# Kernel optimization log

Measured on AMD Instinct MI355X. Metric: run time of the kernel, lower is better.

## Reference

```python
import jax, jax.numpy as jnp
import numpy as np

BN_EPS = 1e-3  # Keras BatchNormalization default epsilon


def batchnorm(x, gamma, beta):
    # axis=2 channel BN with training=True: batch stats over (batch, seq)
    m = jnp.mean(x, axis=(0, 1))
    v = jnp.var(x, axis=(0, 1))
    return gamma * (x - m) * jax.lax.rsqrt(v + BN_EPS) + beta


def setup_inputs() -> dict:
    key = jax.random.key(0)
    ks = jax.random.split(key, 8)
    B, L, Din, D, S = 8, 512, 64, 1024, 2
    s = 0.02
    return {
        "x": jax.random.normal(ks[0], (B, L, Din), jnp.float32),
        "W_embed": jax.random.normal(ks[1], (Din, D), jnp.float32) * s,
        "bn1_gamma": jnp.ones((D,), jnp.float32),
        "bn1_beta": jnp.zeros((D,), jnp.float32),
        "Wq": jax.random.normal(ks[2], (S, D, D), jnp.float32) * s,
        "bq": jnp.zeros((S, D), jnp.float32),
        "Wk": jax.random.normal(ks[3], (S, D, D), jnp.float32) * s,
        "bk": jnp.zeros((S, D), jnp.float32),
        "Wv": jax.random.normal(ks[4], (S, D, D), jnp.float32) * s,
        "bv": jnp.zeros((S, D), jnp.float32),
        "bn_gamma": jnp.ones((S, D), jnp.float32),
        "bn_beta": jnp.zeros((S, D), jnp.float32),
        "Wc1": jax.random.normal(ks[5], (S, D, D), jnp.float32) * s,
        "bc1": jnp.zeros((S, D), jnp.float32),
        "bn2_gamma": jnp.ones((S, D), jnp.float32),
        "bn2_beta": jnp.zeros((S, D), jnp.float32),
        "num_heads": 16,
    }


def reference(x, W_embed, bn1_gamma, bn1_beta, Wq, bq, Wk, bk, Wv, bv,
              bn_gamma, bn_beta, Wc1, bc1, bn2_gamma, bn2_beta, num_heads):
    # embedding: kernel-1 conv1d == matmul, then BN (training stats)
    enc = batchnorm(jnp.einsum('bli,id->bld', x, W_embed), bn1_gamma, bn1_beta)
    S = Wq.shape[0]
    B, L, D = enc.shape
    h = num_heads
    dh = D // h
    scale = 1.0 / (dh ** 0.5)
    for i in range(S):
        # relu-activated Q/K/V projections (Dense(..., activation=relu))
        q = jax.nn.relu(jnp.einsum('bld,de->ble', enc, Wq[i]) + bq[i])
        k = jax.nn.relu(jnp.einsum('bld,de->ble', enc, Wk[i]) + bk[i])
        v = jax.nn.relu(jnp.einsum('bld,de->ble', enc, Wv[i]) + bv[i])
        # split/concat head trick == reshape to [B, L, h, dh]
        qh = q.reshape(B, L, h, dh)
        kh = k.reshape(B, L, h, dh)
        vh = v.reshape(B, L, h, dh)
        scores = jnp.einsum('blhd,bmhd->bhlm', qh, kh) * scale
        attn = jax.nn.softmax(scores, axis=-1)
        out = jnp.einsum('bhlm,bmhd->blhd', attn, vh).reshape(B, L, D)
        enc = batchnorm(out + enc, bn_gamma[i], bn_beta[i])
        # feedforward: source applies conv1 TWICE (conv2 unused) — faithful
        f = jax.nn.relu(jnp.einsum('bld,de->ble', enc, Wc1[i]) + bc1[i])
        f = jax.nn.relu(jnp.einsum('bld,de->ble', f, Wc1[i]) + bc1[i])
        enc = batchnorm(f + enc, bn2_gamma[i], bn2_beta[i])
    return enc
```

## Files before the change

kernel.cpp:

```cpp
#include <hip/hip_runtime.h>
#include <hip/hip_bf16.h>
#include <cstddef>

#define D_MODEL 1024
#define M_ROWS  4096
#define BN_EPS  1e-3f
#define C_EXP2  0.18033688011112042f

typedef __attribute__((ext_vector_type(8))) short short8;
typedef __attribute__((ext_vector_type(4))) short short4v;
typedef __attribute__((ext_vector_type(8))) unsigned short ushortx8;
typedef __attribute__((ext_vector_type(4))) float f32x4;

__device__ __forceinline__ unsigned short f2bf(float f) {
    __hip_bfloat16 h = __float2bfloat16(f);
    return *reinterpret_cast<unsigned short*>(&h);
}
__device__ __forceinline__ float bf2f(unsigned short u) {
    return __uint_as_float(((unsigned)u) << 16);
}

__global__ __launch_bounds__(256)
void embed_kernel(const float* __restrict__ A, const float* __restrict__ W,
                  unsigned short* __restrict__ Sbf, float* __restrict__ accp) {
    __shared__ float As[16][132];
    __shared__ float Bs[16][132];
    const int tid = threadIdx.x;
    const int lane = tid & 63;
    const int tx = tid & 15, ty = tid >> 4;
    const int rowBase = blockIdx.y * 128;
    const int colBase = blockIdx.x * 128;
    float acc[8][8] = {};
    for (int k0 = 0; k0 < 64; k0 += 16) {
        #pragma unroll
        for (int it = 0; it < 2; ++it) {
            int idx = tid + it * 256;
            int r = idx >> 2, c4 = (idx & 3) << 2;
            const float4 v = *reinterpret_cast<const float4*>(
                &A[(size_t)(rowBase + r) * 64 + k0 + c4]);
            As[c4 + 0][r] = v.x; As[c4 + 1][r] = v.y;
            As[c4 + 2][r] = v.z; As[c4 + 3][r] = v.w;
        }
        #pragma unroll
        for (int it = 0; it < 2; ++it) {
            int idx = tid + it * 256;
            int r = idx >> 5, c4 = (idx & 31) << 2;
            const float4 v = *reinterpret_cast<const float4*>(
                &W[(size_t)(k0 + r) * D_MODEL + colBase + c4]);
            *reinterpret_cast<float4*>(&Bs[r][c4]) = v;
        }
        __syncthreads();
        #pragma unroll
        for (int k = 0; k < 16; ++k) {
            const float4 a0 = *reinterpret_cast<const float4*>(&As[k][ty * 8]);
            const float4 a1 = *reinterpret_cast<const float4*>(&As[k][ty * 8 + 4]);
            const float4 b0 = *reinterpret_cast<const float4*>(&Bs[k][tx * 8]);
            const float4 b1 = *reinterpret_cast<const float4*>(&Bs[k][tx * 8 + 4]);
            const float a[8] = {a0.x, a0.y, a0.z, a0.w, a1.x, a1.y, a1.z, a1.w};
            const float b[8] = {b0.x, b0.y, b0.z, b0.w, b1.x, b1.y, b1.z, b1.w};
            #pragma unroll
            for (int i = 0; i < 8; ++i)
                #pragma unroll
                for (int j = 0; j < 8; ++j)
                    acc[i][j] = fmaf(a[i], b[j], acc[i][j]);
        }
        __syncthreads();
    }
    float cs[8] = {}, cq[8] = {};
    #pragma unroll
    for (int i = 0; i < 8; ++i) {
        const int row = rowBase + ty * 8 + i;
        ushortx8 ov;
        #pragma unroll
        for (int j = 0; j < 8; ++j) {
            const float s = acc[i][j];
            ov[j] = f2bf(s);
            cs[j] += s; cq[j] += s * s;
        }
        *reinterpret_cast<ushortx8*>(&Sbf[(size_t)row * D_MODEL + colBase + tx * 8]) = ov;
    }
    #pragma unroll
    for (int j = 0; j < 8; ++j) {
        cs[j] += __shfl_xor(cs[j], 16); cs[j] += __shfl_xor(cs[j], 32);
        cq[j] += __shfl_xor(cq[j], 16); cq[j] += __shfl_xor(cq[j], 32);
    }
    if (lane < 16) {
        #pragma unroll
        for (int j = 0; j < 8; ++j) {
            atomicAdd(&accp[colBase + lane * 8 + j], cs[j]);
            atomicAdd(&accp[D_MODEL + colBase + lane * 8 + j], cq[j]);
        }
    }
}

template<int MODE>
__global__ __launch_bounds__(256)
void gemm_bf16_kernel(const unsigned short* __restrict__ A,
                      const unsigned short* __restrict__ Bt,
                      const float* __restrict__ bias,
                      unsigned short* __restrict__ Cout,
                      const unsigned short* __restrict__ resid,
                      float* __restrict__ accp, int N, int Kd) {
    __shared__ unsigned short As[2][128 * 32];
    __shared__ unsigned short Bs[2][128 * 32];
    const int tid = threadIdx.x;
    const int lane = tid & 63;
    const int w = tid >> 6;
    const int wr = w >> 1, wc = w & 1;
    const int rowBase = blockIdx.y * 128;
    const int colBase = blockIdx.x * 128;

    const int chunk0 = w * 64 + lane;
    const int r0 = chunk0 >> 2;
    const int c0 = (chunk0 & 3) ^ ((r0 >> 1) & 3);
    const int chunk1 = 256 + chunk0;
    const int r1 = chunk1 >> 2;
    const int c1 = (chunk1 & 3) ^ ((r1 >> 1) & 3);
    const size_t aOff0 = (size_t)(rowBase + r0) * Kd + c0 * 8;
    const size_t aOff1 = (size_t)(rowBase + r1) * Kd + c1 * 8;
    const size_t bOff0 = (size_t)(colBase + r0) * Kd + c0 * 8;
    const size_t bOff1 = (size_t)(colBase + r1) * Kd + c1 * 8;
    const int ldsOff0 = (w * 64) * 8;
    const int ldsOff1 = (256 + w * 64) * 8;

    f32x4 acc[4][4];
    #pragma unroll
    for (int m = 0; m < 4; ++m)
        #pragma unroll
        for (int n = 0; n < 4; ++n)
            acc[m][n] = (f32x4){0.f, 0.f, 0.f, 0.f};

    #define STAGE(buf, kt) do {                                                   \
        const int k0_ = (kt) << 5;                                                \
        __builtin_amdgcn_global_load_lds(                                         \
            (const __attribute__((address_space(1))) void*)(A + aOff0 + k0_),     \
            (__attribute__((address_space(3))) void*)(&As[buf][ldsOff0]), 16, 0, 0);\
        __builtin_amdgcn_global_load_lds(                                         \
            (const __attribute__((address_space(1))) void*)(A + aOff1 + k0_),     \
            (__attribute__((address_space(3))) void*)(&As[buf][ldsOff1]), 16, 0, 0);\
        __builtin_amdgcn_global_load_lds(                                         \
            (const __attribute__((address_space(1))) void*)(Bt + bOff0 + k0_),    \
            (__attribute__((address_space(3))) void*)(&Bs[buf][ldsOff0]), 16, 0, 0);\
        __builtin_amdgcn_global_load_lds(                                         \
            (const __attribute__((address_space(1))) void*)(Bt + bOff1 + k0_),    \
            (__attribute__((address_space(3))) void*)(&Bs[buf][ldsOff1]), 16, 0, 0);\
    } while (0)

    const int NT = Kd >> 5;
    STAGE(0, 0);

    const int kb = lane >> 4;
    const int s = kb ^ ((lane >> 1) & 3);
    const int rA = wr * 64 + (lane & 15);
    const int rB = wc * 64 + (lane & 15);

    for (int t = 0; t < NT; ++t) {
        __syncthreads();
        if (t + 1 < NT) STAGE((t + 1) & 1, t + 1);
        const unsigned short* as = As[t & 1];
        const unsigned short* bs = Bs[t & 1];
        short8 a[4], b[4];
        #pragma unroll
        for (int m = 0; m < 4; ++m)
            a[m] = *(const short8*)&as[(rA + m * 16) * 32 + s * 8];
        #pragma unroll
        for (int n = 0; n < 4; ++n)
            b[n] = *(const short8*)&bs[(rB + n * 16) * 32 + s * 8];
        #pragma unroll
        for (int m = 0; m < 4; ++m)
            #pragma unroll
            for (int n = 0; n < 4; ++n)
                acc[m][n] = __builtin_amdgcn_mfma_f32_16x16x32_bf16(
                    a[m], b[n], acc[m][n], 0, 0, 0);
    }
    #undef STAGE

    const int cRow0 = rowBase + wr * 64 + (lane >> 4) * 4;
    const int cCol0 = colBase + wc * 64 + (lane & 15);
    float cs[4] = {}, cq[4] = {};
    #pragma unroll
    for (int n = 0; n < 4; ++n) {
        const int col = cCol0 + n * 16;
        const float bv = bias[col];
        #pragma unroll
        for (int m = 0; m < 4; ++m)
            #pragma unroll
            for (int r = 0; r < 4; ++r) {
                const int row = cRow0 + m * 16 + r;
                float v = fmaxf(acc[m][n][r] + bv, 0.0f);
                if (MODE == 1) {
                    v += bf2f(resid[(size_t)row * N + col]);
                    cs[n] += v; cq[n] += v * v;
                }
                Cout[(size_t)row * N + col] = f2bf(v);
            }
    }
    if (MODE == 1) {
        #pragma unroll
        for (int n = 0; n < 4; ++n) {
            cs[n] += __shfl_xor(cs[n], 16); cs[n] += __shfl_xor(cs[n], 32);
            cq[n] += __shfl_xor(cq[n], 16); cq[n] += __shfl_xor(cq[n], 32);
        }
        if (lane < 16) {
            #pragma unroll
            for (int n = 0; n < 4; ++n) {
                const int col = colBase + wc * 64 + lane + n * 16;
                atomicAdd(&accp[col], cs[n]);
                atomicAdd(&accp[D_MODEL + col], cq[n]);
            }
        }
    }
}

__global__ __launch_bounds__(256)
void transpose_cvt4_kernel(const float* __restrict__ s0, const float* __restrict__ s1,
                           const float* __restrict__ s2, const float* __restrict__ s3,
                           unsigned short* __restrict__ d0, unsigned short* __restrict__ d1,
                           unsigned short* __restrict__ d2, unsigned short* __restrict__ d3) {
    const int z = blockIdx.z;
    const float* src = (z == 0) ? s0 : (z == 1) ? s1 : (z == 2) ? s2 : s3;
    unsigned short* dst = (z == 0) ? d0 : (z == 1) ? d1 : (z == 2) ? d2 : d3;
    __shared__ float T[64][65];
    const int tid = threadIdx.x;
    const int kBase = blockIdx.y * 64;
    const int nBase = blockIdx.x * 64;
    const int rr = tid >> 4;
    const int c4 = (tid & 15) * 4;
    #pragma unroll
    for (int i = 0; i < 4; ++i) {
        const int k = i * 16 + rr;
        const float4 v = *reinterpret_cast<const float4*>(
            &src[(size_t)(kBase + k) * 1024 + nBase + c4]);
        T[k][c4] = v.x; T[k][c4 + 1] = v.y; T[k][c4 + 2] = v.z; T[k][c4 + 3] = v.w;
    }
    __syncthreads();
    #pragma unroll
    for (int i = 0; i < 4; ++i) {
        const int n = i * 16 + rr;
        ushort4 o;
        o.x = f2bf(T[c4 + 0][n]); o.y = f2bf(T[c4 + 1][n]);
        o.z = f2bf(T[c4 + 2][n]); o.w = f2bf(T[c4 + 3][n]);
        *reinterpret_cast<ushort4*>(&dst[(size_t)(nBase + n) * 1024 + kBase + c4]) = o;
    }
}

__global__ __launch_bounds__(256)
void bias_concat_kernel(const float* __restrict__ bq, const float* __restrict__ bk,
                        const float* __restrict__ bv, float* __restrict__ bqkv) {
    const int j = blockIdx.x * 256 + threadIdx.x;
    bqkv[j] = (j < 1024) ? bq[j] : (j < 2048) ? bk[j - 1024] : bv[j - 2048];
}

__global__ __launch_bounds__(256)
void attn_kernel(const unsigned short* __restrict__ QKV,
                 const unsigned short* __restrict__ Ebf,
                 unsigned short* __restrict__ Sbf,
                 float* __restrict__ accp) {
    __shared__ unsigned short Qs[128 * 64];
    __shared__ unsigned short Ks[2][64 * 64];
    __shared__ unsigned short Vt[2][64 * 72];

    const int tid = threadIdx.x;
    const int lane = tid & 63;
    const int w = tid >> 6;
    const int m = lane & 15;
    const int g = lane >> 4;
    const int l7 = lane & 7;
    const int qt = blockIdx.x, hh = blockIdx.y, bb = blockIdx.z;
    const int colB = hh * 64;
    const size_t rowQ = (size_t)bb * 512 + qt * 128;
    const size_t rowKV = (size_t)bb * 512;

    const int vk0 = (tid & 31) * 2;
    const int vcv = tid >> 5;

    #define STAGE_K(buf, kt) do {                                                  \
        const size_t kb_ = rowKV + (size_t)(kt) * 64;                              \
        _Pragma("unroll")                                                          \
        for (int i_ = 0; i_ < 2; ++i_) {                                           \
            const int c_ = w * 128 + i_ * 64 + lane;                               \
            const int r_ = c_ >> 3;                                                \
            const int gc_ = (c_ & 7) ^ (r_ & 7);                                   \
            __builtin_amdgcn_global_load_lds(                                      \
                (const __attribute__((address_space(1))) void*)                    \
                    (QKV + (kb_ + r_) * 3072 + 1024 + colB + gc_ * 8),             \
                (__attribute__((address_space(3))) void*)                          \
                    (&Ks[buf][(w * 128 + i_ * 64) * 8]), 16, 0, 0);                \
        }                                                                          \
    } while (0)

    #define LOAD_V(kt) do {                                                        \
        const size_t kb_ = rowKV + (size_t)(kt) * 64;                              \
        vst0 = *(const ushortx8*)(QKV + (kb_ + vk0) * 3072 + 2048 + colB + vcv * 8);\
        vst1 = *(const ushortx8*)(QKV + (kb_ + vk0 + 1) * 3072 + 2048 + colB + vcv * 8);\
    } while (0)

    #define WRITE_V(buf) do {                                                      \
        _Pragma("unroll")                                                          \
        for (int j_ = 0; j_ < 8; ++j_) {                                           \
            const int d_ = vcv * 8 + j_;                                           \
            unsigned int pk_ = (unsigned int)(unsigned short)vst0[j_] |            \
                               ((unsigned int)(unsigned short)vst1[j_] << 16);     \
            *(unsigned int*)&Vt[buf][d_ * 72 + vk0] = pk_;                         \
        }                                                                          \
    } while (0)

    ushortx8 vst0, vst1;

    #pragma unroll
    for (int i = 0; i < 4; ++i) {
        const int c = w * 256 + i * 64 + lane;
        const int r = c >> 3;
        const int gc = (c & 7) ^ (r & 7);
        __builtin_amdgcn_global_load_lds(
            (const __attribute__((address_space(1))) void*)
                (QKV + (rowQ + r) * 3072 + colB + gc * 8),
            (__attribute__((address_space(3))) void*)
                (&Qs[(w * 256 + i * 64) * 8]), 16, 0, 0);
    }
    STAGE_K(0, 0);
    LOAD_V(0);
    WRITE_V(0);
    __syncthreads();

    short8 qb[2][2];
    #pragma unroll
    for (int nf = 0; nf < 2; ++nf)
        #pragma unroll
        for (int ks = 0; ks < 2; ++ks)
            qb[nf][ks] = *(const short8*)&Qs[(w * 32 + 16 * nf + m) * 64 +
                                             ((g + 4 * ks) ^ l7) * 8];

    f32x4 o[2][4];
    #pragma unroll
    for (int nf = 0; nf < 2; ++nf)
        #pragma unroll
        for (int dn = 0; dn < 4; ++dn)
            o[nf][dn] = (f32x4){0.f, 0.f, 0.f, 0.f};
    float mr[2] = {-1e30f, -1e30f};
    float lsm[2] = {0.f, 0.f};

    for (int kt = 0; kt < 8; ++kt) {
        const int cur = kt & 1, nxt = cur ^ 1;
        if (kt < 7) { STAGE_K(nxt, kt + 1); LOAD_V(kt + 1); }

        f32x4 st[4][2];
        #pragma unroll
        for (int mf = 0; mf < 4; ++mf)
            #pragma unroll
            for (int nf = 0; nf < 2; ++nf)
                st[mf][nf] = (f32x4){0.f, 0.f, 0.f, 0.f};
        #pragma unroll
        for (int ks = 0; ks < 2; ++ks) {
            short8 a[4];
            #pragma unroll
            for (int mf = 0; mf < 4; ++mf)
                a[mf] = *(const short8*)&Ks[cur][(m + 16 * mf) * 64 +
                                                 ((g + 4 * ks) ^ l7) * 8];
            #pragma unroll
            for (int mf = 0; mf < 4; ++mf)
                #pragma unroll
                for (int nf = 0; nf < 2; ++nf)
                    st[mf][nf] = __builtin_amdgcn_mfma_f32_16x16x32_bf16(
                        a[mf], qb[nf][ks], st[mf][nf], 0, 0, 0);
        }

        float pmax[2];
        #pragma unroll
        for (int nf = 0; nf < 2; ++nf) {
            float mx = st[0][nf][0];
            #pragma unroll
            for (int mf = 0; mf < 4; ++mf)
                #pragma unroll
                for (int r = 0; r < 4; ++r)
                    mx = fmaxf(mx, st[mf][nf][r]);
            mx = fmaxf(mx, __shfl_xor(mx, 16));
            mx = fmaxf(mx, __shfl_xor(mx, 32));
            pmax[nf] = mx;
        }
        const int need = (pmax[0] - mr[0] > 64.f) || (pmax[1] - mr[1] > 64.f);
        if (__any(need)) {
            float al[2];
            #pragma unroll
            for (int nf = 0; nf < 2; ++nf) {
                const float mn = fmaxf(mr[nf], pmax[nf]);
                al[nf] = exp2f((mr[nf] - mn) * C_EXP2);
                lsm[nf] *= al[nf];
                mr[nf] = mn;
            }
            #pragma unroll
            for (int nf = 0; nf < 2; ++nf)
                #pragma unroll
                for (int r = 0; r < 4; ++r) {
                    const float av = __shfl(al[nf], 4 * g + r);
                    #pragma unroll
                    for (int dn = 0; dn < 4; ++dn)
                        o[nf][dn][r] *= av;
                }
        }

        float pf[2][4][4];
        #pragma unroll
        for (int nf = 0; nf < 2; ++nf) {
            const float mc = mr[nf] * C_EXP2;
            float ls = 0.f;
            #pragma unroll
            for (int mf = 0; mf < 4; ++mf)
                #pragma unroll
                for (int r = 0; r < 4; ++r) {
                    const float p = exp2f(fmaf(st[mf][nf][r], C_EXP2, -mc));
                    pf[nf][mf][r] = p;
                    ls += p;
                }
            ls += __shfl_xor(ls, 16);
            ls += __shfl_xor(ls, 32);
            lsm[nf] += ls;
        }

        if (kt < 7) WRITE_V(nxt);

        short8 pb[2][2];
        #pragma unroll
        for (int nf = 0; nf < 2; ++nf)
            #pragma unroll
            for (int ks = 0; ks < 2; ++ks)
                #pragma unroll
                for (int j = 0; j < 8; ++j)
                    pb[nf][ks][j] = (short)f2bf(pf[nf][(j >> 2) + 2 * ks][j & 3]);

        #pragma unroll
        for (int ks = 0; ks < 2; ++ks) {
            short8 vb[4];
            #pragma unroll
            for (int dn = 0; dn < 4; ++dn) {
                const int d = m + 16 * dn;
                const short4v lo = *(const short4v*)&Vt[cur][d * 72 + 4 * g + 32 * ks];
                const short4v hi = *(const short4v*)&Vt[cur][d * 72 + 4 * g + 16 + 32 * ks];
                vb[dn] = __builtin_shufflevector(lo, hi, 0, 1, 2, 3, 4, 5, 6, 7);
            }
            #pragma unroll
            for (int nf = 0; nf < 2; ++nf)
                #pragma unroll
                for (int dn = 0; dn < 4; ++dn)
                    o[nf][dn] = __builtin_amdgcn_mfma_f32_16x16x32_bf16(
                        pb[nf][ks], vb[dn], o[nf][dn], 0, 0, 0);
        }
        __syncthreads();
    }

    float cs[4] = {}, cq[4] = {};
    #pragma unroll
    for (int nf = 0; nf < 2; ++nf) {
        const float inv = 1.0f / lsm[nf];
        #pragma unroll
        for (int r = 0; r < 4; ++r) {
            const float sc = __shfl(inv, 4 * g + r);
            const size_t row = rowQ + w * 32 + 16 * nf + 4 * g + r;
            #pragma unroll
            for (int dn = 0; dn < 4; ++dn) {
                const int ch = colB + 16 * dn + m;
                const float sv = o[nf][dn][r] * sc + bf2f(Ebf[row * D_MODEL + ch]);
                Sbf[row * D_MODEL + ch] = f2bf(sv);
                cs[dn] += sv; cq[dn] += sv * sv;
            }
        }
    }
    #pragma unroll
    for (int dn = 0; dn < 4; ++dn) {
        cs[dn] += __shfl_xor(cs[dn], 16); cs[dn] += __shfl_xor(cs[dn], 32);
        cq[dn] += __shfl_xor(cq[dn], 16); cq[dn] += __shfl_xor(cq[dn], 32);
    }
    if (lane < 16) {
        #pragma unroll
        for (int dn = 0; dn < 4; ++dn) {
            atomicAdd(&accp[colB + 16 * dn + lane], cs[dn]);
            atomicAdd(&accp[D_MODEL + colB + 16 * dn + lane], cq[dn]);
        }
    }
    #undef STAGE_K
    #undef LOAD_V
    #undef WRITE_V
}

__global__ __launch_bounds__(256)
void bn_final_kernel(const float* __restrict__ accp, const float* __restrict__ gamma,
                     const float* __restrict__ beta, float* __restrict__ coef) {
    const int c = blockIdx.x * 256 + threadIdx.x;
    const float mean = accp[c] * (1.0f / 4096.0f);
    const float var = accp[D_MODEL + c] * (1.0f / 4096.0f) - mean * mean;
    const float s = gamma[c] * rsqrtf(var + BN_EPS);
    coef[c] = s;
    coef[D_MODEL + c] = beta[c] - mean * s;
}

template<bool FINAL>
__global__ __launch_bounds__(256)
void bn_apply_kernel(const unsigned short* __restrict__ S, const float* __restrict__ coef,
                     unsigned short* __restrict__ Ebf, float* __restrict__ outF) {
    const int idx = blockIdx.x * 256 + threadIdx.x;
    const int c8 = (idx & 127) << 3;
    const ushortx8 sv = *(const ushortx8*)&S[(size_t)idx * 8];
    const float4 a0 = *(const float4*)&coef[c8];
    const float4 a1 = *(const float4*)&coef[c8 + 4];
    const float4 b0 = *(const float4*)&coef[D_MODEL + c8];
    const float4 b1 = *(const float4*)&coef[D_MODEL + c8 + 4];
    const float a[8] = {a0.x, a0.y, a0.z, a0.w, a1.x, a1.y, a1.z, a1.w};
    const float b[8] = {b0.x, b0.y, b0.z, b0.w, b1.x, b1.y, b1.z, b1.w};
    float o[8];
    #pragma unroll
    for (int j = 0; j < 8; ++j) o[j] = fmaf(bf2f(sv[j]), a[j], b[j]);
    if (FINAL) {
        *reinterpret_cast<float4*>(&outF[(size_t)idx * 8]) =
            make_float4(o[0], o[1], o[2], o[3]);
        *reinterpret_cast<float4*>(&outF[(size_t)idx * 8 + 4]) =
            make_float4(o[4], o[5], o[6], o[7]);
    } else {
        ushortx8 e;
        #pragma unroll
        for (int j = 0; j < 8; ++j) e[j] = f2bf(o[j]);
        *reinterpret_cast<ushortx8*>(&Ebf[(size_t)idx * 8]) = e;
    }
}

extern "C" void kernel_launch(void* const* d_in, const int* in_sizes, int n_in,
                              void* d_out, int out_size, void* d_ws, size_t ws_size,
                              hipStream_t stream) {
    const float* x       = (const float*)d_in[0];
    const float* W_embed = (const float*)d_in[1];
    const float* bn1_g   = (const float*)d_in[2];
    const float* bn1_b   = (const float*)d_in[3];
    const float* Wq      = (const float*)d_in[4];
    const float* bq      = (const float*)d_in[5];
    const float* Wk      = (const float*)d_in[6];
    const float* bk      = (const float*)d_in[7];
    const float* Wv      = (const float*)d_in[8];
    const float* bv      = (const float*)d_in[9];
    const float* bng     = (const float*)d_in[10];
    const float* bnb     = (const float*)d_in[11];
    const float* Wc1     = (const float*)d_in[12];
    const float* bc1     = (const float*)d_in[13];
    const float* bn2g    = (const float*)d_in[14];
    const float* bn2b    = (const float*)d_in[15];

    const size_t NBUF = (size_t)M_ROWS * D_MODEL;
    char* ws = (char*)d_ws;
    float* accum = (float*)ws;
    float* coef  = accum + 5 * 2048;
    float* bqkv  = coef + 2048;
    unsigned short* Ebf   = (unsigned short*)(bqkv + 3072);
    unsigned short* Sbf   = Ebf + NBUF;
    unsigned short* QKVbf = Sbf + NBUF;
    unsigned short* F1bf  = QKVbf;
    unsigned short* Wtqkv = QKVbf + (size_t)M_ROWS * 3072;
    unsigned short* Wtc1  = Wtqkv + (size_t)3072 * 1024;
    float* outF = (float*)d_out;

    hipMemsetAsync(accum, 0, 5 * 2048 * sizeof(float), stream);

    embed_kernel<<<dim3(8, 32), 256, 0, stream>>>(x, W_embed, Sbf, accum);
    bn_final_kernel<<<4, 256, 0, stream>>>(accum, bn1_g, bn1_b, coef);
    bn_apply_kernel<false><<<2048, 256, 0, stream>>>(Sbf, coef, Ebf, nullptr);

    for (int i = 0; i < 2; ++i) {
        const size_t wo = (size_t)i * D_MODEL * D_MODEL;
        const size_t bo = (size_t)i * D_MODEL;
        float* accA = accum + (1 + 2 * i) * 2048;
        float* accF = accum + (2 + 2 * i) * 2048;

        transpose_cvt4_kernel<<<dim3(16, 16, 4), 256, 0, stream>>>(
            Wq + wo, Wk + wo, Wv + wo, Wc1 + wo,
            Wtqkv, Wtqkv + (size_t)1024 * 1024, Wtqkv + (size_t)2048 * 1024, Wtc1);
        bias_concat_kernel<<<12, 256, 0, stream>>>(bq + bo, bk + bo, bv + bo, bqkv);

        gemm_bf16_kernel<0><<<dim3(24, 32), 256, 0, stream>>>(
            Ebf, Wtqkv, bqkv, QKVbf, nullptr, nullptr, 3072, 1024);
        attn_kernel<<<dim3(4, 16, 8), 256, 0, stream>>>(QKVbf, Ebf, Sbf, accA);
        bn_final_kernel<<<4, 256, 0, stream>>>(accA, bng + bo, bnb + bo, coef);
        bn_apply_kernel<false><<<2048, 256, 0, stream>>>(Sbf, coef, Ebf, nullptr);

        gemm_bf16_kernel<0><<<dim3(8, 32), 256, 0, stream>>>(
            Ebf, Wtc1, bc1 + bo, F1bf, nullptr, nullptr, 1024, 1024);
        gemm_bf16_kernel<1><<<dim3(8, 32), 256, 0, stream>>>(
            F1bf, Wtc1, bc1 + bo, Sbf, Ebf, accF, 1024, 1024);
        bn_final_kernel<<<4, 256, 0, stream>>>(accF, bn2g + bo, bn2b + bo, coef);
        if (i == 0)
            bn_apply_kernel<false><<<2048, 256, 0, stream>>>(Sbf, coef, Ebf, nullptr);
        else
            bn_apply_kernel<true><<<2048, 256, 0, stream>>>(Sbf, coef, nullptr, outF);
    }
}
```

Before: 318.3 us.

## Consolidate launches: bf16 MFMA embed, fused BN finalize, batched weight prep

Replaces the fp32 embed GEMM with a bf16 MFMA GEMM mode (MODE 2) fed by a new prep kernel that converts x and transposes W_embed. That prep kernel also zeroes the accumulators, which removes the memset. Both layers' weights are now transposed in a single launch, the bias concat kernel is dropped by selecting q/k/v bias pointers per column in the epilogue, and the BN finalize step is folded into bn_apply. The attention kernel gains setprio around its MFMAs, tree reductions for max and sum, and packed bf16 conversion. These changes cut roughly nine launches, but the embed input is now rounded to bf16 and every bn_apply thread recomputes rsqrt.

```diff
diff --git a/kernel.cpp b/kernel.cpp
--- a/kernel.cpp
+++ b/kernel.cpp
@@ -6,6 +6,7 @@
 #define M_ROWS  4096
 #define BN_EPS  1e-3f
 #define C_EXP2  0.18033688011112042f
+#define INV_N   (1.0f / 4096.0f)
 
 typedef __attribute__((ext_vector_type(8))) short short8;
 typedef __attribute__((ext_vector_type(4))) short short4v;
@@ -19,85 +20,18 @@
 __device__ __forceinline__ float bf2f(unsigned short u) {
     return __uint_as_float(((unsigned)u) << 16);
 }
-
-__global__ __launch_bounds__(256)
-void embed_kernel(const float* __restrict__ A, const float* __restrict__ W,
-                  unsigned short* __restrict__ Sbf, float* __restrict__ accp) {
-    __shared__ float As[16][132];
-    __shared__ float Bs[16][132];
-    const int tid = threadIdx.x;
-    const int lane = tid & 63;
-    const int tx = tid & 15, ty = tid >> 4;
-    const int rowBase = blockIdx.y * 128;
-    const int colBase = blockIdx.x * 128;
-    float acc[8][8] = {};
-    for (int k0 = 0; k0 < 64; k0 += 16) {
-        #pragma unroll
-        for (int it = 0; it < 2; ++it) {
-            int idx = tid + it * 256;
-            int r = idx >> 2, c4 = (idx & 3) << 2;
-            const float4 v = *reinterpret_cast<const float4*>(
-                &A[(size_t)(rowBase + r) * 64 + k0 + c4]);
-            As[c4 + 0][r] = v.x; As[c4 + 1][r] = v.y;
-            As[c4 + 2][r] = v.z; As[c4 + 3][r] = v.w;
-        }
-        #pragma unroll
-        for (int it = 0; it < 2; ++it) {
-            int idx = tid + it * 256;
-            int r = idx >> 5, c4 = (idx & 31) << 2;
-            const float4 v = *reinterpret_cast<const float4*>(
-                &W[(size_t)(k0 + r) * D_MODEL + colBase + c4]);
-            *reinterpret_cast<float4*>(&Bs[r][c4]) = v;
-        }
-        __syncthreads();
-        #pragma unroll
-        for (int k = 0; k < 16; ++k) {
-            const float4 a0 = *reinterpret_cast<const float4*>(&As[k][ty * 8]);
-            const float4 a1 = *reinterpret_cast<const float4*>(&As[k][ty * 8 + 4]);
-            const float4 b0 = *reinterpret_cast<const float4*>(&Bs[k][tx * 8]);
-            const float4 b1 = *reinterpret_cast<const float4*>(&Bs[k][tx * 8 + 4]);
-            const float a[8] = {a0.x, a0.y, a0.z, a0.w, a1.x, a1.y, a1.z, a1.w};
-            const float b[8] = {b0.x, b0.y, b0.z, b0.w, b1.x, b1.y, b1.z, b1.w};
-            #pragma unroll
-            for (int i = 0; i < 8; ++i)
-                #pragma unroll
-                for (int j = 0; j < 8; ++j)
-                    acc[i][j] = fmaf(a[i], b[j], acc[i][j]);
-        }
-        __syncthreads();
-    }
-    float cs[8] = {}, cq[8] = {};
-    #pragma unroll
-    for (int i = 0; i < 8; ++i) {
-        const int row = rowBase + ty * 8 + i;
-        ushortx8 ov;
-        #pragma unroll
-        for (int j = 0; j < 8; ++j) {
-            const float s = acc[i][j];
-            ov[j] = f2bf(s);
-            cs[j] += s; cq[j] += s * s;
-        }
-        *reinterpret_cast<ushortx8*>(&Sbf[(size_t)row * D_MODEL + colBase + tx * 8]) = ov;
-    }
-    #pragma unroll
-    for (int j = 0; j < 8; ++j) {
-        cs[j] += __shfl_xor(cs[j], 16); cs[j] += __shfl_xor(cs[j], 32);
-        cq[j] += __shfl_xor(cq[j], 16); cq[j] += __shfl_xor(cq[j], 32);
-    }
-    if (lane < 16) {
-        #pragma unroll
-        for (int j = 0; j < 8; ++j) {
-            atomicAdd(&accp[colBase + lane * 8 + j], cs[j]);
-            atomicAdd(&accp[D_MODEL + colBase + lane * 8 + j], cq[j]);
-        }
-    }
+__device__ __forceinline__ unsigned int cvt_pk_bf16(float lo, float hi) {
+    unsigned int r;
+    asm volatile("v_cvt_pk_bf16_f32 %0, %1, %2" : "=v"(r) : "v"(lo), "v"(hi));
+    return r;
 }
 
 template<int MODE>
 __global__ __launch_bounds__(256)
 void gemm_bf16_kernel(const unsigned short* __restrict__ A,
                       const unsigned short* __restrict__ Bt,
-                      const float* __restrict__ bias,
+                      const float* __restrict__ b0, const float* __restrict__ b1,
+                      const float* __restrict__ b2,
                       unsigned short* __restrict__ Cout,
                       const unsigned short* __restrict__ resid,
                       float* __restrict__ accp, int N, int Kd) {
@@ -181,21 +115,24 @@
     #pragma unroll
     for (int n = 0; n < 4; ++n) {
         const int col = cCol0 + n * 16;
-        const float bv = bias[col];
+        float bv = 0.0f;
+        if (MODE != 2) {
+            const float* bp = (col < 1024) ? b0 : (col < 2048) ? b1 : b2;
+            bv = bp[col & 1023];
+        }
         #pragma unroll
         for (int m = 0; m < 4; ++m)
             #pragma unroll
             for (int r = 0; r < 4; ++r) {
                 const int row = cRow0 + m * 16 + r;
-                float v = fmaxf(acc[m][n][r] + bv, 0.0f);
-                if (MODE == 1) {
-                    v += bf2f(resid[(size_t)row * N + col]);
-                    cs[n] += v; cq[n] += v * v;
-                }
+                float v = acc[m][n][r];
+                if (MODE != 2) v = fmaxf(v + bv, 0.0f);
+                if (MODE == 1) v += bf2f(resid[(size_t)row * N + col]);
+                if (MODE != 0) { cs[n] += v; cq[n] += v * v; }
                 Cout[(size_t)row * N + col] = f2bf(v);
             }
     }
-    if (MODE == 1) {
+    if (MODE != 0) {
         #pragma unroll
         for (int n = 0; n < 4; ++n) {
             cs[n] += __shfl_xor(cs[n], 16); cs[n] += __shfl_xor(cs[n], 32);
@@ -213,13 +150,19 @@
 }
 
 __global__ __launch_bounds__(256)
-void transpose_cvt4_kernel(const float* __restrict__ s0, const float* __restrict__ s1,
-                           const float* __restrict__ s2, const float* __restrict__ s3,
-                           unsigned short* __restrict__ d0, unsigned short* __restrict__ d1,
-                           unsigned short* __restrict__ d2, unsigned short* __restrict__ d3) {
+void prep_weights_kernel(const float* __restrict__ Wq, const float* __restrict__ Wk,
+                         const float* __restrict__ Wv, const float* __restrict__ Wc1,
+                         unsigned short* __restrict__ Wtqkv,
+                         unsigned short* __restrict__ Wtc1) {
     const int z = blockIdx.z;
-    const float* src = (z == 0) ? s0 : (z == 1) ? s1 : (z == 2) ? s2 : s3;
-    unsigned short* dst = (z == 0) ? d0 : (z == 1) ? d1 : (z == 2) ? d2 : d3;
+    const int layer = z >> 2, typ = z & 3;
+    const size_t wo = (size_t)layer * 1048576;
+    const float* src;
+    unsigned short* dst;
+    if (typ == 0)      { src = Wq + wo;  dst = Wtqkv + layer * 3145728; }
+    else if (typ == 1) { src = Wk + wo;  dst = Wtqkv + layer * 3145728 + 1048576; }
+    else if (typ == 2) { src = Wv + wo;  dst = Wtqkv + layer * 3145728 + 2097152; }
+    else               { src = Wc1 + wo; dst = Wtc1 + layer * 1048576; }
     __shared__ float T[64][65];
     const int tid = threadIdx.x;
     const int kBase = blockIdx.y * 64;
@@ -245,10 +188,44 @@
 }
 
 __global__ __launch_bounds__(256)
-void bias_concat_kernel(const float* __restrict__ bq, const float* __restrict__ bk,
-                        const float* __restrict__ bv, float* __restrict__ bqkv) {
-    const int j = blockIdx.x * 256 + threadIdx.x;
-    bqkv[j] = (j < 1024) ? bq[j] : (j < 2048) ? bk[j - 1024] : bv[j - 2048];
+void prep_misc_kernel(const float* __restrict__ x, const float* __restrict__ Wemb,
+                      unsigned short* __restrict__ xbf,
+                      unsigned short* __restrict__ Wembt,
+                      float* __restrict__ accum) {
+    const int b = blockIdx.x;
+    const int tid = threadIdx.x;
+    if (b < 128) {
+        const size_t base = (size_t)b * 2048 + tid * 8;
+        const float4 v0 = *reinterpret_cast<const float4*>(&x[base]);
+        const float4 v1 = *reinterpret_cast<const float4*>(&x[base + 4]);
+        ushortx8 o;
+        o[0] = f2bf(v0.x); o[1] = f2bf(v0.y); o[2] = f2bf(v0.z); o[3] = f2bf(v0.w);
+        o[4] = f2bf(v1.x); o[5] = f2bf(v1.y); o[6] = f2bf(v1.z); o[7] = f2bf(v1.w);
+        *reinterpret_cast<ushortx8*>(&xbf[base]) = o;
+    } else if (b < 144) {
+        __shared__ float T[64][65];
+        const int nBase = (b - 128) * 64;
+        const int rr = tid >> 4;
+        const int c4 = (tid & 15) * 4;
+        #pragma unroll
+        for (int i = 0; i < 4; ++i) {
+            const int k = i * 16 + rr;
+            const float4 v = *reinterpret_cast<const float4*>(
+                &Wemb[(size_t)k * 1024 + nBase + c4]);
+            T[k][c4] = v.x; T[k][c4 + 1] = v.y; T[k][c4 + 2] = v.z; T[k][c4 + 3] = v.w;
+        }
+        __syncthreads();
+        #pragma unroll
+        for (int i = 0; i < 4; ++i) {
+            const int n = i * 16 + rr;
+            ushort4 o;
+            o.x = f2bf(T[c4 + 0][n]); o.y = f2bf(T[c4 + 1][n]);
+            o.z = f2bf(T[c4 + 2][n]); o.w = f2bf(T[c4 + 3][n]);
+            *reinterpret_cast<ushort4*>(&Wembt[(size_t)(nBase + n) * 64 + c4]) = o;
+        }
+    } else {
+        for (int j = tid; j < 5 * 2048; j += 256) accum[j] = 0.0f;
+    }
 }
 
 __global__ __launch_bounds__(256)
@@ -357,23 +334,28 @@
             for (int mf = 0; mf < 4; ++mf)
                 a[mf] = *(const short8*)&Ks[cur][(m + 16 * mf) * 64 +
                                                  ((g + 4 * ks) ^ l7) * 8];
+            __builtin_amdgcn_s_setprio(1);
             #pragma unroll
             for (int mf = 0; mf < 4; ++mf)
                 #pragma unroll
                 for (int nf = 0; nf < 2; ++nf)
                     st[mf][nf] = __builtin_amdgcn_mfma_f32_16x16x32_bf16(
                         a[mf], qb[nf][ks], st[mf][nf], 0, 0, 0);
+            __builtin_amdgcn_s_setprio(0);
         }
 
         float pmax[2];
         #pragma unroll
         for (int nf = 0; nf < 2; ++nf) {
-            float mx = st[0][nf][0];
-            #pragma unroll
-            for (int mf = 0; mf < 4; ++mf)
-                #pragma unroll
-                for (int r = 0; r < 4; ++r)
-                    mx = fmaxf(mx, st[mf][nf][r]);
+            float a0 = fmaxf(fmaxf(st[0][nf][0], st[0][nf][1]),
+                             fmaxf(st[0][nf][2], st[0][nf][3]));
+            float a1 = fmaxf(fmaxf(st[1][nf][0], st[1][nf][1]),
+                             fmaxf(st[1][nf][2], st[1][nf][3]));
+            float a2 = fmaxf(fmaxf(st[2][nf][0], st[2][nf][1]),
+                             fmaxf(st[2][nf][2], st[2][nf][3]));
+            float a3 = fmaxf(fmaxf(st[3][nf][0], st[3][nf][1]),
+                             fmaxf(st[3][nf][2], st[3][nf][3]));
+            float mx = fmaxf(fmaxf(a0, a1), fmaxf(a2, a3));
             mx = fmaxf(mx, __shfl_xor(mx, 16));
             mx = fmaxf(mx, __shfl_xor(mx, 32));
             pmax[nf] = mx;
@@ -403,15 +385,18 @@
         #pragma unroll
         for (int nf = 0; nf < 2; ++nf) {
             const float mc = mr[nf] * C_EXP2;
-            float ls = 0.f;
-            #pragma unroll
-            for (int mf = 0; mf < 4; ++mf)
-                #pragma unroll
-                for (int r = 0; r < 4; ++r) {
-                    const float p = exp2f(fmaf(st[mf][nf][r], C_EXP2, -mc));
-                    pf[nf][mf][r] = p;
-                    ls += p;
-                }
+            float s0 = 0.f, s1 = 0.f, s2 = 0.f, s3 = 0.f;
+            #pragma unroll
+            for (int mf = 0; mf < 4; ++mf) {
+                float p0 = exp2f(fmaf(st[mf][nf][0], C_EXP2, -mc));
+                float p1 = exp2f(fmaf(st[mf][nf][1], C_EXP2, -mc));
+                float p2 = exp2f(fmaf(st[mf][nf][2], C_EXP2, -mc));
+                float p3 = exp2f(fmaf(st[mf][nf][3], C_EXP2, -mc));
+                pf[nf][mf][0] = p0; pf[nf][mf][1] = p1;
+                pf[nf][mf][2] = p2; pf[nf][mf][3] = p3;
+                s0 += p0; s1 += p1; s2 += p2; s3 += p3;
+            }
+            float ls = (s0 + s1) + (s2 + s3);
             ls += __shfl_xor(ls, 16);
             ls += __shfl_xor(ls, 32);
             lsm[nf] += ls;
@@ -423,10 +408,14 @@
         #pragma unroll
         for (int nf = 0; nf < 2; ++nf)
             #pragma unroll
-            for (int ks = 0; ks < 2; ++ks)
-                #pragma unroll
-                for (int j = 0; j < 8; ++j)
-                    pb[nf][ks][j] = (short)f2bf(pf[nf][(j >> 2) + 2 * ks][j & 3]);
+            for (int ks = 0; ks < 2; ++ks) {
+                union { unsigned int u[4]; short8 s; } cv;
+                cv.u[0] = cvt_pk_bf16(pf[nf][2 * ks][0], pf[nf][2 * ks][1]);
+                cv.u[1] = cvt_pk_bf16(pf[nf][2 * ks][2], pf[nf][2 * ks][3]);
+                cv.u[2] = cvt_pk_bf16(pf[nf][2 * ks + 1][0], pf[nf][2 * ks + 1][1]);
+                cv.u[3] = cvt_pk_bf16(pf[nf][2 * ks + 1][2], pf[nf][2 * ks + 1][3]);
+                pb[nf][ks] = cv.s;
+            }
 
         #pragma unroll
         for (int ks = 0; ks < 2; ++ks) {
@@ -438,12 +427,14 @@
                 const short4v hi = *(const short4v*)&Vt[cur][d * 72 + 4 * g + 16 + 32 * ks];
                 vb[dn] = __builtin_shufflevector(lo, hi, 0, 1, 2, 3, 4, 5, 6, 7);
             }
+            __builtin_amdgcn_s_setprio(1);
             #pragma unroll
             for (int nf = 0; nf < 2; ++nf)
                 #pragma unroll
                 for (int dn = 0; dn < 4; ++dn)
                     o[nf][dn] = __builtin_amdgcn_mfma_f32_16x16x32_bf16(
                         pb[nf][ks], vb[dn], o[nf][dn], 0, 0, 0);
+            __builtin_amdgcn_s_setprio(0);
         }
         __syncthreads();
     }
@@ -482,43 +473,49 @@
     #undef WRITE_V
 }
 
-__global__ __launch_bounds__(256)
-void bn_final_kernel(const float* __restrict__ accp, const float* __restrict__ gamma,
-                     const float* __restrict__ beta, float* __restrict__ coef) {
-    const int c = blockIdx.x * 256 + threadIdx.x;
-    const float mean = accp[c] * (1.0f / 4096.0f);
-    const float var = accp[D_MODEL + c] * (1.0f / 4096.0f) - mean * mean;
-    const float s = gamma[c] * rsqrtf(var + BN_EPS);
-    coef[c] = s;
-    coef[D_MODEL + c] = beta[c] - mean * s;
-}
-
 template<bool FINAL>
 __global__ __launch_bounds__(256)
-void bn_apply_kernel(const unsigned short* __restrict__ S, const float* __restrict__ coef,
-                     unsigned short* __restrict__ Ebf, float* __restrict__ outF) {
+void bn_apply_kernel(const unsigned short* __restrict__ S,
+                     const float* __restrict__ accum,
+                     const float* __restrict__ gamma,
+                     const float* __restrict__ beta,
+                     unsigned short* __restrict__ Ebf,
+                     float* __restrict__ outF) {
     const int idx = blockIdx.x * 256 + threadIdx.x;
     const int c8 = (idx & 127) << 3;
     const ushortx8 sv = *(const ushortx8*)&S[(size_t)idx * 8];
-    const float4 a0 = *(const float4*)&coef[c8];
-    const float4 a1 = *(const float4*)&coef[c8 + 4];
-    const float4 b0 = *(const float4*)&coef[D_MODEL + c8];
-    const float4 b1 = *(const float4*)&coef[D_MODEL + c8 + 4];
-    const float a[8] = {a0.x, a0.y, a0.z, a0.w, a1.x, a1.y, a1.z, a1.w};
-    const float b[8] = {b0.x, b0.y, b0.z, b0.w, b1.x, b1.y, b1.z, b1.w};
+    const float4 s0 = *(const float4*)&accum[c8];
+    const float4 s1 = *(const float4*)&accum[c8 + 4];
+    const float4 q0 = *(const float4*)&accum[D_MODEL + c8];
+    const float4 q1 = *(const float4*)&accum[D_MODEL + c8 + 4];
+    const float4 g0 = *(const float4*)&gamma[c8];
+    const float4 g1 = *(const float4*)&gamma[c8 + 4];
+    const float4 t0 = *(const float4*)&beta[c8];
+    const float4 t1 = *(const float4*)&beta[c8 + 4];
+    const float ss[8] = {s0.x, s0.y, s0.z, s0.w, s1.x, s1.y, s1.z, s1.w};
+    const float qq[8] = {q0.x, q0.y, q0.z, q0.w, q1.x, q1.y, q1.z, q1.w};
+    const float gg[8] = {g0.x, g0.y, g0.z, g0.w, g1.x, g1.y, g1.z, g1.w};
+    const float tt[8] = {t0.x, t0.y, t0.z, t0.w, t1.x, t1.y, t1.z, t1.w};
     float o[8];
     #pragma unroll
-    for (int j = 0; j < 8; ++j) o[j] = fmaf(bf2f(sv[j]), a[j], b[j]);
+    for (int j = 0; j < 8; ++j) {
+        const float mean = ss[j] * INV_N;
+        const float var = qq[j] * INV_N - mean * mean;
+        const float a = gg[j] * rsqrtf(var + BN_EPS);
+        o[j] = fmaf(bf2f(sv[j]), a, tt[j] - mean * a);
+    }
     if (FINAL) {
         *reinterpret_cast<float4*>(&outF[(size_t)idx * 8]) =
             make_float4(o[0], o[1], o[2], o[3]);
         *reinterpret_cast<float4*>(&outF[(size_t)idx * 8 + 4]) =
             make_float4(o[4], o[5], o[6], o[7]);
     } else {
-        ushortx8 e;
-        #pragma unroll
-        for (int j = 0; j < 8; ++j) e[j] = f2bf(o[j]);
-        *reinterpret_cast<ushortx8*>(&Ebf[(size_t)idx * 8]) = e;
+        union { unsigned int u[4]; ushortx8 s; } cv;
+        cv.u[0] = cvt_pk_bf16(o[0], o[1]);
+        cv.u[1] = cvt_pk_bf16(o[2], o[3]);
+        cv.u[2] = cvt_pk_bf16(o[4], o[5]);
+        cv.u[3] = cvt_pk_bf16(o[6], o[7]);
+        *reinterpret_cast<ushortx8*>(&Ebf[(size_t)idx * 8]) = cv.s;
     }
 }
 
@@ -545,47 +542,50 @@
     const size_t NBUF = (size_t)M_ROWS * D_MODEL;
     char* ws = (char*)d_ws;
     float* accum = (float*)ws;
-    float* coef  = accum + 5 * 2048;
-    float* bqkv  = coef + 2048;
-    unsigned short* Ebf   = (unsigned short*)(bqkv + 3072);
+    unsigned short* xbf   = (unsigned short*)(accum + 5 * 2048);
+    unsigned short* Wembt = xbf + 262144;
+    unsigned short* Ebf   = Wembt + 65536;
     unsigned short* Sbf   = Ebf + NBUF;
     unsigned short* QKVbf = Sbf + NBUF;
     unsigned short* F1bf  = QKVbf;
     unsigned short* Wtqkv = QKVbf + (size_t)M_ROWS * 3072;
-    unsigned short* Wtc1  = Wtqkv + (size_t)3072 * 1024;
+    unsigned short* Wtc1  = Wtqkv + 2 * (size_t)3145728;
     float* outF = (float*)d_out;
 
-    hipMemsetAsync(accum, 0, 5 * 2048 * sizeof(float), stream);
-
-    embed_kernel<<<dim3(8, 32), 256, 0, stream>>>(x, W_embed, Sbf, accum);
-    bn_final_kernel<<<4, 256, 0, stream>>>(accum, bn1_g, bn1_b, coef);
-    bn_apply_kernel<false><<<2048, 256, 0, stream>>>(Sbf, coef, Ebf, nullptr);
+    prep_misc_kernel<<<145, 256, 0, stream>>>(x, W_embed, xbf, Wembt, accum);
+    prep_weights_kernel<<<dim3(16, 16, 8), 256, 0, stream>>>(Wq, Wk, Wv, Wc1,
+                                                             Wtqkv, Wtc1);
+
+    gemm_bf16_kernel<2><<<dim3(8, 32), 256, 0, stream>>>(
+        xbf, Wembt, nullptr, nullptr, nullptr, Sbf, nullptr, accum, 1024, 64);
+    bn_apply_kernel<false><<<2048, 256, 0, stream>>>(Sbf, accum, bn1_g, bn1_b,
+                                                     Ebf, nullptr);
 
     for (int i = 0; i < 2; ++i) {
-        const size_t wo = (size_t)i * D_MODEL * D_MODEL;
         const size_t bo = (size_t)i * D_MODEL;
         float* accA = accum + (1 + 2 * i) * 2048;
         float* accF = accum + (2 + 2 * i) * 2048;
-
-        transpose_cvt4_kernel<<<dim3(16, 16, 4), 256, 0, stream>>>(
-            Wq + wo, Wk + wo, Wv + wo, Wc1 + wo,
-            Wtqkv, Wtqkv + (size_t)1024 * 1024, Wtqkv + (size_t)2048 * 1024, Wtc1);
-        bias_concat_kernel<<<12, 256, 0, stream>>>(bq + bo, bk + bo, bv + bo, bqkv);
+        const unsigned short* WtqkvL = Wtqkv + (size_t)i * 3145728;
+        const unsigned short* Wtc1L  = Wtc1 + (size_t)i * 1048576;
 
         gemm_bf16_kernel<0><<<dim3(24, 32), 256, 0, stream>>>(
-            Ebf, Wtqkv, bqkv, QKVbf, nullptr, nullptr, 3072, 1024);
+            Ebf, WtqkvL, bq + bo, bk + bo, bv + bo, QKVbf, nullptr, nullptr,
+            3072, 1024);
         attn_kernel<<<dim3(4, 16, 8), 256, 0, stream>>>(QKVbf, Ebf, Sbf, accA);
-        bn_final_kernel<<<4, 256, 0, stream>>>(accA, bng + bo, bnb + bo, coef);
-        bn_apply_kernel<false><<<2048, 256, 0, stream>>>(Sbf, coef, Ebf, nullptr);
+        bn_apply_kernel<false><<<2048, 256, 0, stream>>>(Sbf, accA, bng + bo,
+                                                         bnb + bo, Ebf, nullptr);
 
         gemm_bf16_kernel<0><<<dim3(8, 32), 256, 0, stream>>>(
-            Ebf, Wtc1, bc1 + bo, F1bf, nullptr, nullptr, 1024, 1024);
+            Ebf, Wtc1L, bc1 + bo, bc1 + bo, bc1 + bo, F1bf, nullptr, nullptr,
+            1024, 1024);
         gemm_bf16_kernel<1><<<dim3(8, 32), 256, 0, stream>>>(
-            F1bf, Wtc1, bc1 + bo, Sbf, Ebf, accF, 1024, 1024);
-        bn_final_kernel<<<4, 256, 0, stream>>>(accF, bn2g + bo, bn2b + bo, coef);
+            F1bf, Wtc1L, bc1 + bo, bc1 + bo, bc1 + bo, Sbf, Ebf, accF,
+            1024, 1024);
         if (i == 0)
-            bn_apply_kernel<false><<<2048, 256, 0, stream>>>(Sbf, coef, Ebf, nullptr);
+            bn_apply_kernel<false><<<2048, 256, 0, stream>>>(Sbf, accF, bn2g + bo,
+                                                             bn2b + bo, Ebf, nullptr);
         else
-            bn_apply_kernel<true><<<2048, 256, 0, stream>>>(Sbf, coef, nullptr, outF);
-    }
-}
+            bn_apply_kernel<true><<<2048, 256, 0, stream>>>(Sbf, accF, bn2g + bo,
+                                                            bn2b + bo, nullptr, outF);
+    }
+}
```

New measurement: 275.3 us, median of 2. 13.5% less time.
